# Kernel optimization log

Hardware: AMD Instinct MI355X
Metric: run time of the kernel (lower is better)

The kernel has to match this reference:

```python
import jax, jax.numpy as jnp
import numpy as np

NUM_HEADS = 8
IN_CH = 256  # C per branch; x has 2*C channels
DHW = (16, 16, 16)


def _proj(w, b, feat):
    # 1x1x1 Conv3d == per-voxel linear over channels. w: [Co, Ci], feat: [B, Ci, D, H, W]
    return jnp.einsum('oc,bcdhw->bodhw', w, feat) + b[None, :, None, None, None]


def _rope(n, dim):
    # matches rotary_embedding: returns [dim, n]
    inv_freq = 1.0 / (10000.0 ** (jnp.arange(0, dim, 2, dtype=jnp.float32) / dim))
    pos = jnp.linspace(-1.0, 1.0, n)
    sinusoid = pos[:, None] * inv_freq[None, :]          # [n, dim//2]
    emb = jnp.concatenate([jnp.sin(sinusoid), jnp.cos(sinusoid)], axis=-1)  # [n, dim]
    return emb.T                                          # [dim, n]


def setup_inputs() -> dict:
    key = jax.random.key(0)
    ks = jax.random.split(key, 5)
    D, H, W = DHW
    C = IN_CH
    s = 0.05
    return {
        'x': jax.random.normal(ks[0], (1, 2 * C, D, H, W), dtype=jnp.float32),
        'wq': jax.random.normal(ks[1], (C, C), dtype=jnp.float32) * s,
        'bq': jnp.zeros((C,), jnp.float32),
        'wk': jax.random.normal(ks[2], (C, C), dtype=jnp.float32) * s,
        'bk': jnp.zeros((C,), jnp.float32),
        'wv': jax.random.normal(ks[3], (C, C), dtype=jnp.float32) * s,
        'bv': jnp.zeros((C,), jnp.float32),
        'wo': jax.random.normal(ks[4], (2 * C, C), dtype=jnp.float32) * s,
        'bo': jnp.zeros((2 * C,), jnp.float32),
    }


def reference(x, wq, bq, wk, bk, wv, bv, wo, bo):
    qf, kvf = jnp.split(x, 2, axis=1)          # each [B, C, D, H, W]
    B, C, D, H, W = qf.shape
    hd = C // NUM_HEADS
    N = D * H * W
    q = _proj(wq, bq, qf).reshape(B, NUM_HEADS, hd, N)
    k = _proj(wk, bk, kvf).reshape(B, NUM_HEADS, hd, N)
    v = _proj(wv, bv, kvf).reshape(B, NUM_HEADS, hd, N)
    pe = _rope(N, hd)                           # [hd, N]
    q = q * pe[None, None]
    k = k * pe[None, None]
    attn = jnp.einsum('bhcn,bhcm->bhnm', q, k)  # note: no 1/sqrt(d) scaling, as in source
    attn = jax.nn.softmax(attn, axis=-1)
    out = jnp.einsum('bhnm,bhcm->bhcn', attn, v).reshape(B, C, D, H, W)
    return _proj(wo, bo, out + qf)              # [B, 2C, D, H, W]
```

## Files before the change

### kernel.cpp

```cpp
#include <hip/hip_runtime.h>
#include <hip/hip_bf16.h>

#define CIN 256
#define NV 4096
#define NHEAD 8
#define HD 32
#define NSPLIT 4
#define KSPAN (NV / NSPLIT)
#define KTILE 128
#define LOG2E 1.44269504088896340736f
#define LOG2_10K_16 0.8304820237218405f

typedef __attribute__((ext_vector_type(8))) short short8;
typedef __attribute__((ext_vector_type(4))) float f32x4;

static __device__ __forceinline__ unsigned short f2bf(float f) {
    union { float f; unsigned u; } v; v.f = f;
    unsigned r = v.u + 0x7fffu + ((v.u >> 16) & 1u);
    return (unsigned short)(r >> 16);
}
static __device__ __forceinline__ unsigned pk_bf2(float x0, float x1) {
    return __builtin_amdgcn_perm(__float_as_uint(x1), __float_as_uint(x0),
                                 0x07060302u);
}
static __device__ __forceinline__ float bflo(unsigned u) {
    return __uint_as_float(u << 16);
}
static __device__ __forceinline__ float bfhi(unsigned u) {
    return __uint_as_float(u & 0xffff0000u);
}

__global__ __launch_bounds__(256) void conv_w(
    const float* __restrict__ wq, const float* __restrict__ wk,
    const float* __restrict__ wv, const float* __restrict__ wo,
    unsigned short* __restrict__ Wb)
{
    int i = (blockIdx.x * 256 + threadIdx.x) * 4;
    if (i >= 327680) return;
    const float* src;
    int off = i;
    if (i < 65536) { src = wq; }
    else if (i < 131072) { src = wk; off = i - 65536; }
    else if (i < 196608) { src = wv; off = i - 131072; }
    else { src = wo; off = i - 196608; }
    float4 v = *(const float4*)&src[off];
    unsigned short pk[4] = {f2bf(v.x), f2bf(v.y), f2bf(v.z), f2bf(v.w)};
    *(uint2*)&Wb[i] = *(uint2*)pk;
}

__global__ __launch_bounds__(512) void qkv_fused(
    const float* __restrict__ x, const unsigned short* __restrict__ Wb,
    const float* __restrict__ bq, const float* __restrict__ bk,
    const float* __restrict__ bv,
    unsigned short* __restrict__ Qbf, unsigned short* __restrict__ Kbf,
    unsigned short* __restrict__ Vbf)
{
    const int which = blockIdx.z;
    const unsigned short* Wp = Wb + (size_t)which * 65536;
    const float* Bp = (which == 0) ? bq : (which == 1) ? bk : bv;
    const int cbase = (which == 0) ? 0 : CIN;

    const int n0 = blockIdx.x * 32;
    const int m0 = blockIdx.y * 128;
    const int t = threadIdx.x;

    __shared__ __align__(16) unsigned short Sbuf[32 * 264];

    {
        const int n = t & 31, cg = t >> 5;
#pragma unroll 4
        for (int cc = 0; cc < 16; cc += 2) {
            const int c = cg * 16 + cc;
            size_t off = (size_t)(cbase + c) * NV + n0 + n;
            *(unsigned*)&Sbuf[n * 264 + c] = pk_bf2(x[off], x[off + NV]);
        }
    }
    __syncthreads();

    const int w = t >> 6;
    const int lane = t & 63;
    const int ln = lane & 15;
    const int quad = lane >> 4;
    const int M = m0 + w * 16 + ln;

    f32x4 acc[2] = {};
    const unsigned short* Wrow = &Wp[(size_t)M * 256 + quad * 8];
    for (int k0 = 0; k0 < 256; k0 += 32) {
        short8 a = *(const short8*)&Wrow[k0];
        short8 b[2];
#pragma unroll
        for (int nt = 0; nt < 2; ++nt)
            b[nt] = *(const short8*)&Sbuf[(nt * 16 + ln) * 264 + k0 + quad * 8];
        if (which == 2) {
#pragma unroll
            for (int nt = 0; nt < 2; ++nt)
                acc[nt] = __builtin_amdgcn_mfma_f32_16x16x32_bf16(
                    b[nt], a, acc[nt], 0, 0, 0);
        } else {
#pragma unroll
            for (int nt = 0; nt < 2; ++nt)
                acc[nt] = __builtin_amdgcn_mfma_f32_16x16x32_bf16(
                    a, b[nt], acc[nt], 0, 0, 0);
        }
    }
    __syncthreads();

    if (which == 2) {
        const int cl = w * 16 + ln;
        const float bias = Bp[m0 + cl];
#pragma unroll
        for (int nt = 0; nt < 2; ++nt) {
            unsigned short pk4[4];
#pragma unroll
            for (int r = 0; r < 4; ++r) pk4[r] = f2bf(acc[nt][r] + bias);
            *(uint2*)&Sbuf[cl * 40 + nt * 16 + quad * 4] = *(uint2*)pk4;
        }
        __syncthreads();
        {
            const int cl2 = t >> 2, q = t & 3;
            uint2 lo = *(const uint2*)&Sbuf[cl2 * 40 + q * 4];
            uint2 hi = *(const uint2*)&Sbuf[cl2 * 40 + 16 + q * 4];
            uint4 v;
            v.x = lo.x; v.y = lo.y; v.z = hi.x; v.w = hi.y;
            *(uint4*)&Vbf[(size_t)(m0 + cl2) * NV + n0 + q * 8] = v;
        }
    } else {
        const int mb = m0 + w * 16 + quad * 4;
        const int cb = mb & 31;
        const float qscale = (which == 0) ? LOG2E : 1.0f;
        float bias[4], invf[4];
#pragma unroll
        for (int r = 0; r < 4; ++r) {
            bias[r] = Bp[mb + r];
            invf[r] = __builtin_amdgcn_exp2f(
                -(float)((cb + r) & 15) * LOG2_10K_16);
        }
        const bool use_sin = (cb < 16);
        const int ml = w * 16 + quad * 4;
#pragma unroll
        for (int nt = 0; nt < 2; ++nt) {
            const int n = n0 + nt * 16 + ln;
            const float pos = (float)n * (2.0f / 4095.0f) - 1.0f;
#pragma unroll
            for (int r = 0; r < 4; ++r) {
                float ang = pos * invf[r];
                float f = (use_sin ? __sinf(ang) : __cosf(ang)) * qscale;
                Sbuf[(nt * 16 + ln) * 264 + ml + r] =
                    f2bf((acc[nt][r] + bias[r]) * f);
            }
        }
        __syncthreads();
        unsigned short* dst = (which == 0) ? Qbf : Kbf;
        const int h0 = m0 >> 5;
        {
            const int hh = t >> 7;
            const int n = (t >> 2) & 31;
            const int cw = t & 3;
            uint4 v = *(const uint4*)&Sbuf[n * 264 + hh * 32 + cw * 8];
            *(uint4*)&dst[((size_t)(h0 + hh) * NV + n0 + n) * HD + cw * 8] = v;
        }
    }
}

__global__ __launch_bounds__(256, 4) void attn_mfma(
    const unsigned short* __restrict__ Qbf,
    const unsigned short* __restrict__ Kbf,
    const unsigned short* __restrict__ Vbf,
    unsigned short* __restrict__ Opartb, float* __restrict__ Lpart)
{
    const int h = blockIdx.y;
    const int q0 = blockIdx.x * 64;
    const int z = blockIdx.z;
    const int kbase = z * KSPAN;
    const int t = threadIdx.x;
    const int w = t >> 6;
    const int lane = t & 63;
    const int ln = lane & 15;
    const int quad = lane >> 4;

    __shared__ __align__(16) unsigned short Ks[2][2 * 2048];
    __shared__ __align__(16) unsigned short Vs[2][2 * 2048];

    const short8 qa = *(const short8*)
        &Qbf[((size_t)h * NV + q0 + w * 16 + ln) * HD + quad * 8];

    const unsigned short* Kh = Kbf + (size_t)h * NV * HD;
    const unsigned short* Vh = Vbf + (size_t)h * HD * NV;

    const int cv = t >> 3;
    const unsigned short* gsrcV = Vh + (size_t)cv * NV + ((t & 7) ^ (cv & 7)) * 8;
    const int kv = t >> 2;
    const unsigned short* gsrcK =
        Kh + (size_t)kv * HD + ((t & 3) ^ (kv & 3)) * 8;

    f32x4 oacc[2] = {};
    f32x4 lacc = {};
    const short vone = (short)0x3F80;
    const short8 vones = {vone, vone, vone, vone, vone, vone, vone, vone};

#pragma unroll
    for (int sblk = 0; sblk < 2; ++sblk) {
        __builtin_amdgcn_global_load_lds(
            (const __attribute__((address_space(1))) unsigned int*)(gsrcK +
                (size_t)(kbase + sblk * 64) * HD),
            (__attribute__((address_space(3))) unsigned int*)
                (&Ks[0][sblk * 2048] + t * 8), 16, 0, 0);
        __builtin_amdgcn_global_load_lds(
            (const __attribute__((address_space(1))) unsigned int*)(gsrcV +
                kbase + sblk * 64),
            (__attribute__((address_space(3))) unsigned int*)
                (&Vs[0][sblk * 2048] + t * 8), 16, 0, 0);
    }
    __syncthreads();

    const int sgk = (quad ^ (ln & 3)) * 8;
    for (int i = 0; i < KSPAN / KTILE; ++i) {
        const int kb = kbase + i * KTILE;
        const int buf = i & 1;

        if (i + 1 < KSPAN / KTILE) {
#pragma unroll
            for (int sblk = 0; sblk < 2; ++sblk) {
                __builtin_amdgcn_global_load_lds(
                    (const __attribute__((address_space(1))) unsigned int*)
                        (gsrcK + (size_t)(kb + KTILE + sblk * 64) * HD),
                    (__attribute__((address_space(3))) unsigned int*)
                        (&Ks[buf ^ 1][sblk * 2048] + t * 8), 16, 0, 0);
                __builtin_amdgcn_global_load_lds(
                    (const __attribute__((address_space(1))) unsigned int*)
                        (gsrcV + kb + KTILE + sblk * 64),
                    (__attribute__((address_space(3))) unsigned int*)
                        (&Vs[buf ^ 1][sblk * 2048] + t * 8), 16, 0, 0);
            }
        }

#pragma unroll
        for (int sblk = 0; sblk < 2; ++sblk) {
            f32x4 s[4];
#pragma unroll
            for (int ct = 0; ct < 4; ++ct) {
                const short8 kf = *(const short8*)
                    &Ks[buf][sblk * 2048 + (ct * 16 + ln) * 32 + sgk];
                f32x4 z4 = {0.f, 0.f, 0.f, 0.f};
                s[ct] = __builtin_amdgcn_mfma_f32_16x16x32_bf16(kf, qa, z4,
                                                                0, 0, 0);
            }

            float p[4][4];
#pragma unroll
            for (int ct = 0; ct < 4; ++ct)
#pragma unroll
                for (int r = 0; r < 4; ++r)
                    p[ct][r] = __builtin_amdgcn_exp2f(s[ct][r]);

#pragma unroll
            for (int h2 = 0; h2 < 2; ++h2) {
                short8 pa;
                unsigned* pau = (unsigned*)&pa;
                pau[0] = pk_bf2(p[2 * h2][0], p[2 * h2][1]);
                pau[1] = pk_bf2(p[2 * h2][2], p[2 * h2][3]);
                pau[2] = pk_bf2(p[2 * h2 + 1][0], p[2 * h2 + 1][1]);
                pau[3] = pk_bf2(p[2 * h2 + 1][2], p[2 * h2 + 1][3]);
                lacc = __builtin_amdgcn_mfma_f32_16x16x32_bf16(pa, vones, lacc,
                                                               0, 0, 0);
#pragma unroll
                for (int ctile = 0; ctile < 2; ++ctile) {
                    const int cA = ctile * 16 + ln;
                    const short8 vb = *(const short8*)
                        &Vs[buf][sblk * 2048 + cA * 64 +
                                 (((h2 * 4 + quad) ^ (cA & 7)) * 8)];
                    oacc[ctile] = __builtin_amdgcn_mfma_f32_16x16x32_bf16(
                        pa, vb, oacc[ctile], 0, 0, 0);
                }
            }
        }
        __syncthreads();
    }

    unsigned short* Oz = Opartb + (size_t)z * CIN * NV;
    float* Lz = Lpart + (size_t)z * NHEAD * NV;
    if (ln == 0) {
#pragma unroll
        for (int r = 0; r < 4; ++r)
            Lz[(size_t)h * NV + q0 + w * 16 + quad * 4 + r] = lacc[r];
    }
#pragma unroll
    for (int ctile = 0; ctile < 2; ++ctile) {
        uint2 st;
        st.x = pk_bf2(oacc[ctile][0], oacc[ctile][1]);
        st.y = pk_bf2(oacc[ctile][2], oacc[ctile][3]);
        *(uint2*)&Oz[(size_t)(h * HD + ctile * 16 + ln) * NV + q0 + w * 16 +
                     quad * 4] = st;
    }
}

__global__ __launch_bounds__(512) void out_fused(
    const float* __restrict__ x,
    const unsigned short* __restrict__ Opartb,
    const float* __restrict__ Lpart,
    const unsigned short* __restrict__ Wob, const float* __restrict__ bo,
    float* __restrict__ out)
{
    const int n0 = blockIdx.x * 32;
    const int m0 = blockIdx.y * 128;
    const int t = threadIdx.x;

    __shared__ __align__(16) unsigned short Ys[32 * 264];

    {
        const int n2 = (t & 15) * 2;
        const int grp = t >> 4;
        const int h = grp >> 2;
        const size_t lo = (size_t)h * NV + n0 + n2;
        float l0 = 0.f, l1 = 0.f;
#pragma unroll
        for (int zz = 0; zz < NSPLIT; ++zz) {
            l0 += Lpart[(size_t)zz * NHEAD * NV + lo];
            l1 += Lpart[(size_t)zz * NHEAD * NV + lo + 1];
        }
        const float rl0 = __builtin_amdgcn_rcpf(l0);
        const float rl1 = __builtin_amdgcn_rcpf(l1);
#pragma unroll
        for (int i = 0; i < 8; ++i) {
            const int c = grp * 8 + i;
            size_t off = (size_t)c * NV + n0 + n2;
            float s0 = 0.f, s1 = 0.f;
#pragma unroll
            for (int zz = 0; zz < NSPLIT; ++zz) {
                unsigned o = *(const unsigned*)&Opartb[(size_t)zz * CIN * NV + off];
                s0 += bflo(o);
                s1 += bfhi(o);
            }
            float2 x2 = *(const float2*)&x[off];
            Ys[n2 * 264 + c] = f2bf(s0 * rl0 + x2.x);
            Ys[(n2 + 1) * 264 + c] = f2bf(s1 * rl1 + x2.y);
        }
    }
    __syncthreads();

    const int w = t >> 6;
    const int lane = t & 63;
    const int ln = lane & 15;
    const int quad = lane >> 4;
    const int M = m0 + w * 16 + ln;

    const unsigned short* Wrow = &Wob[(size_t)M * 256 + quad * 8];
    f32x4 acc[2] = {};
    for (int k0 = 0; k0 < 256; k0 += 32) {
        short8 a = *(const short8*)&Wrow[k0];
        short8 b[2];
#pragma unroll
        for (int nt = 0; nt < 2; ++nt)
            b[nt] = *(const short8*)&Ys[(nt * 16 + ln) * 264 + k0 + quad * 8];
#pragma unroll
        for (int nt = 0; nt < 2; ++nt)
            acc[nt] = __builtin_amdgcn_mfma_f32_16x16x32_bf16(
                a, b[nt], acc[nt], 0, 0, 0);
    }

    const int mb = m0 + w * 16 + quad * 4;
    float bias[4];
#pragma unroll
    for (int r = 0; r < 4; ++r) bias[r] = bo[mb + r];
#pragma unroll
    for (int nt = 0; nt < 2; ++nt)
#pragma unroll
        for (int r = 0; r < 4; ++r)
            out[(size_t)(mb + r) * NV + n0 + nt * 16 + ln] =
                acc[nt][r] + bias[r];
}

extern "C" void kernel_launch(void* const* d_in, const int* in_sizes, int n_in,
                              void* d_out, int out_size, void* d_ws,
                              size_t ws_size, hipStream_t stream)
{
    const float* x  = (const float*)d_in[0];
    const float* wq = (const float*)d_in[1];
    const float* bq = (const float*)d_in[2];
    const float* wk = (const float*)d_in[3];
    const float* bk = (const float*)d_in[4];
    const float* wv = (const float*)d_in[5];
    const float* bv = (const float*)d_in[6];
    const float* wo = (const float*)d_in[7];
    const float* bo = (const float*)d_in[8];
    float* out = (float*)d_out;

    unsigned short* Wb  = (unsigned short*)d_ws;
    unsigned short* Qbf = Wb + 327680;
    unsigned short* Kbf = Qbf + (size_t)CIN * NV;
    unsigned short* Vbf = Kbf + (size_t)CIN * NV;
    float* Lpart = (float*)(Vbf + (size_t)CIN * NV);
    unsigned short* Opartb =
        (unsigned short*)(Lpart + NSPLIT * (size_t)NHEAD * NV);

    conv_w<<<dim3(320), 256, 0, stream>>>(wq, wk, wv, wo, Wb);
    qkv_fused<<<dim3(128, 2, 3), 512, 0, stream>>>(
        x, Wb, bq, bk, bv, Qbf, Kbf, Vbf);
    attn_mfma<<<dim3(NV / 64, NHEAD, NSPLIT), 256, 0, stream>>>(
        Qbf, Kbf, Vbf, Opartb, Lpart);
    out_fused<<<dim3(128, 4), 512, 0, stream>>>(
        x, Opartb, Lpart, Wb + 196608, bo, out);
}
```

Baseline: 120.9 us.

## Fuse weight bf16 conversion into GEMMs and double query tile per attention block

```diff
diff --git a/kernel.cpp b/kernel.cpp
--- a/kernel.cpp
+++ b/kernel.cpp
@@ -30,33 +30,16 @@
     return __uint_as_float(u & 0xffff0000u);
 }
 
-__global__ __launch_bounds__(256) void conv_w(
-    const float* __restrict__ wq, const float* __restrict__ wk,
-    const float* __restrict__ wv, const float* __restrict__ wo,
-    unsigned short* __restrict__ Wb)
-{
-    int i = (blockIdx.x * 256 + threadIdx.x) * 4;
-    if (i >= 327680) return;
-    const float* src;
-    int off = i;
-    if (i < 65536) { src = wq; }
-    else if (i < 131072) { src = wk; off = i - 65536; }
-    else if (i < 196608) { src = wv; off = i - 131072; }
-    else { src = wo; off = i - 196608; }
-    float4 v = *(const float4*)&src[off];
-    unsigned short pk[4] = {f2bf(v.x), f2bf(v.y), f2bf(v.z), f2bf(v.w)};
-    *(uint2*)&Wb[i] = *(uint2*)pk;
-}
-
 __global__ __launch_bounds__(512) void qkv_fused(
-    const float* __restrict__ x, const unsigned short* __restrict__ Wb,
-    const float* __restrict__ bq, const float* __restrict__ bk,
-    const float* __restrict__ bv,
+    const float* __restrict__ x,
+    const float* __restrict__ wq, const float* __restrict__ bq,
+    const float* __restrict__ wk, const float* __restrict__ bk,
+    const float* __restrict__ wv, const float* __restrict__ bv,
     unsigned short* __restrict__ Qbf, unsigned short* __restrict__ Kbf,
     unsigned short* __restrict__ Vbf)
 {
     const int which = blockIdx.z;
-    const unsigned short* Wp = Wb + (size_t)which * 65536;
+    const float* Wp = (which == 0) ? wq : (which == 1) ? wk : wv;
     const float* Bp = (which == 0) ? bq : (which == 1) ? bk : bv;
     const int cbase = (which == 0) ? 0 : CIN;
 
@@ -84,9 +67,16 @@
     const int M = m0 + w * 16 + ln;
 
     f32x4 acc[2] = {};
-    const unsigned short* Wrow = &Wp[(size_t)M * 256 + quad * 8];
+    const float* Wrow = &Wp[(size_t)M * 256 + quad * 8];
     for (int k0 = 0; k0 < 256; k0 += 32) {
-        short8 a = *(const short8*)&Wrow[k0];
+        float4 a0 = *(const float4*)&Wrow[k0];
+        float4 a1 = *(const float4*)&Wrow[k0 + 4];
+        short8 a;
+        unsigned* au = (unsigned*)&a;
+        au[0] = pk_bf2(a0.x, a0.y);
+        au[1] = pk_bf2(a0.z, a0.w);
+        au[2] = pk_bf2(a1.x, a1.y);
+        au[3] = pk_bf2(a1.z, a1.w);
         short8 b[2];
 #pragma unroll
         for (int nt = 0; nt < 2; ++nt)
@@ -169,7 +159,7 @@
     unsigned short* __restrict__ Opartb, float* __restrict__ Lpart)
 {
     const int h = blockIdx.y;
-    const int q0 = blockIdx.x * 64;
+    const int q0 = blockIdx.x * 128;
     const int z = blockIdx.z;
     const int kbase = z * KSPAN;
     const int t = threadIdx.x;
@@ -181,8 +171,11 @@
     __shared__ __align__(16) unsigned short Ks[2][2 * 2048];
     __shared__ __align__(16) unsigned short Vs[2][2 * 2048];
 
-    const short8 qa = *(const short8*)
-        &Qbf[((size_t)h * NV + q0 + w * 16 + ln) * HD + quad * 8];
+    short8 qa[2];
+#pragma unroll
+    for (int s = 0; s < 2; ++s)
+        qa[s] = *(const short8*)
+            &Qbf[((size_t)h * NV + q0 + s * 64 + w * 16 + ln) * HD + quad * 8];
 
     const unsigned short* Kh = Kbf + (size_t)h * NV * HD;
     const unsigned short* Vh = Vbf + (size_t)h * HD * NV;
@@ -191,10 +184,10 @@
     const unsigned short* gsrcV = Vh + (size_t)cv * NV + ((t & 7) ^ (cv & 7)) * 8;
     const int kv = t >> 2;
     const unsigned short* gsrcK =
-        Kh + (size_t)kv * HD + ((t & 3) ^ (kv & 3)) * 8;
-
-    f32x4 oacc[2] = {};
-    f32x4 lacc = {};
+        Kh + (size_t)kv * HD + ((t & 3) ^ ((kv >> 1) & 3)) * 8;
+
+    f32x4 oacc[2][2] = {};
+    f32x4 lacc[2] = {};
     const short vone = (short)0x3F80;
     const short8 vones = {vone, vone, vone, vone, vone, vone, vone, vone};
 
@@ -213,7 +206,7 @@
     }
     __syncthreads();
 
-    const int sgk = (quad ^ (ln & 3)) * 8;
+    const int sgk = (quad ^ ((ln >> 1) & 3)) * 8;
     for (int i = 0; i < KSPAN / KTILE; ++i) {
         const int kb = kbase + i * KTILE;
         const int buf = i & 1;
@@ -236,41 +229,62 @@
 
 #pragma unroll
         for (int sblk = 0; sblk < 2; ++sblk) {
-            f32x4 s[4];
-#pragma unroll
-            for (int ct = 0; ct < 4; ++ct) {
-                const short8 kf = *(const short8*)
+            short8 kfr[4];
+#pragma unroll
+            for (int ct = 0; ct < 4; ++ct)
+                kfr[ct] = *(const short8*)
                     &Ks[buf][sblk * 2048 + (ct * 16 + ln) * 32 + sgk];
-                f32x4 z4 = {0.f, 0.f, 0.f, 0.f};
-                s[ct] = __builtin_amdgcn_mfma_f32_16x16x32_bf16(kf, qa, z4,
-                                                                0, 0, 0);
+
+            unsigned paP[2][8];
+#pragma unroll
+            for (int s = 0; s < 2; ++s) {
+                f32x4 sv[4];
+#pragma unroll
+                for (int ct = 0; ct < 4; ++ct) {
+                    f32x4 z4 = {0.f, 0.f, 0.f, 0.f};
+                    sv[ct] = __builtin_amdgcn_mfma_f32_16x16x32_bf16(
+                        kfr[ct], qa[s], z4, 0, 0, 0);
+                }
+                float p[4][4];
+#pragma unroll
+                for (int ct = 0; ct < 4; ++ct)
+#pragma unroll
+                    for (int r = 0; r < 4; ++r)
+                        p[ct][r] = __builtin_amdgcn_exp2f(sv[ct][r]);
+#pragma unroll
+                for (int h2 = 0; h2 < 2; ++h2) {
+                    paP[s][h2 * 4 + 0] = pk_bf2(p[2 * h2][0], p[2 * h2][1]);
+                    paP[s][h2 * 4 + 1] = pk_bf2(p[2 * h2][2], p[2 * h2][3]);
+                    paP[s][h2 * 4 + 2] =
+                        pk_bf2(p[2 * h2 + 1][0], p[2 * h2 + 1][1]);
+                    paP[s][h2 * 4 + 3] =
+                        pk_bf2(p[2 * h2 + 1][2], p[2 * h2 + 1][3]);
+                }
             }
 
-            float p[4][4];
-#pragma unroll
-            for (int ct = 0; ct < 4; ++ct)
-#pragma unroll
-                for (int r = 0; r < 4; ++r)
-                    p[ct][r] = __builtin_amdgcn_exp2f(s[ct][r]);
-
 #pragma unroll
             for (int h2 = 0; h2 < 2; ++h2) {
-                short8 pa;
-                unsigned* pau = (unsigned*)&pa;
-                pau[0] = pk_bf2(p[2 * h2][0], p[2 * h2][1]);
-                pau[1] = pk_bf2(p[2 * h2][2], p[2 * h2][3]);
-                pau[2] = pk_bf2(p[2 * h2 + 1][0], p[2 * h2 + 1][1]);
-                pau[3] = pk_bf2(p[2 * h2 + 1][2], p[2 * h2 + 1][3]);
-                lacc = __builtin_amdgcn_mfma_f32_16x16x32_bf16(pa, vones, lacc,
-                                                               0, 0, 0);
+                short8 pa[2];
+#pragma unroll
+                for (int s = 0; s < 2; ++s) {
+                    unsigned* pau = (unsigned*)&pa[s];
+                    pau[0] = paP[s][h2 * 4 + 0];
+                    pau[1] = paP[s][h2 * 4 + 1];
+                    pau[2] = paP[s][h2 * 4 + 2];
+                    pau[3] = paP[s][h2 * 4 + 3];
+                    lacc[s] = __builtin_amdgcn_mfma_f32_16x16x32_bf16(
+                        pa[s], vones, lacc[s], 0, 0, 0);
+                }
 #pragma unroll
                 for (int ctile = 0; ctile < 2; ++ctile) {
                     const int cA = ctile * 16 + ln;
                     const short8 vb = *(const short8*)
                         &Vs[buf][sblk * 2048 + cA * 64 +
                                  (((h2 * 4 + quad) ^ (cA & 7)) * 8)];
-                    oacc[ctile] = __builtin_amdgcn_mfma_f32_16x16x32_bf16(
-                        pa, vb, oacc[ctile], 0, 0, 0);
+#pragma unroll
+                    for (int s = 0; s < 2; ++s)
+                        oacc[s][ctile] = __builtin_amdgcn_mfma_f32_16x16x32_bf16(
+                            pa[s], vb, oacc[s][ctile], 0, 0, 0);
                 }
             }
         }
@@ -279,18 +293,22 @@
 
     unsigned short* Oz = Opartb + (size_t)z * CIN * NV;
     float* Lz = Lpart + (size_t)z * NHEAD * NV;
-    if (ln == 0) {
-#pragma unroll
-        for (int r = 0; r < 4; ++r)
-            Lz[(size_t)h * NV + q0 + w * 16 + quad * 4 + r] = lacc[r];
-    }
-#pragma unroll
-    for (int ctile = 0; ctile < 2; ++ctile) {
-        uint2 st;
-        st.x = pk_bf2(oacc[ctile][0], oacc[ctile][1]);
-        st.y = pk_bf2(oacc[ctile][2], oacc[ctile][3]);
-        *(uint2*)&Oz[(size_t)(h * HD + ctile * 16 + ln) * NV + q0 + w * 16 +
-                     quad * 4] = st;
+#pragma unroll
+    for (int s = 0; s < 2; ++s) {
+        const int qs = q0 + s * 64 + w * 16;
+        if (ln == 0) {
+#pragma unroll
+            for (int r = 0; r < 4; ++r)
+                Lz[(size_t)h * NV + qs + quad * 4 + r] = lacc[s][r];
+        }
+#pragma unroll
+        for (int ctile = 0; ctile < 2; ++ctile) {
+            uint2 st;
+            st.x = pk_bf2(oacc[s][ctile][0], oacc[s][ctile][1]);
+            st.y = pk_bf2(oacc[s][ctile][2], oacc[s][ctile][3]);
+            *(uint2*)&Oz[(size_t)(h * HD + ctile * 16 + ln) * NV + qs +
+                         quad * 4] = st;
+        }
     }
 }
 
@@ -298,7 +316,7 @@
     const float* __restrict__ x,
     const unsigned short* __restrict__ Opartb,
     const float* __restrict__ Lpart,
-    const unsigned short* __restrict__ Wob, const float* __restrict__ bo,
+    const float* __restrict__ wo, const float* __restrict__ bo,
     float* __restrict__ out)
 {
     const int n0 = blockIdx.x * 32;
@@ -344,10 +362,17 @@
     const int quad = lane >> 4;
     const int M = m0 + w * 16 + ln;
 
-    const unsigned short* Wrow = &Wob[(size_t)M * 256 + quad * 8];
+    const float* Wrow = &wo[(size_t)M * 256 + quad * 8];
     f32x4 acc[2] = {};
     for (int k0 = 0; k0 < 256; k0 += 32) {
-        short8 a = *(const short8*)&Wrow[k0];
+        float4 a0 = *(const float4*)&Wrow[k0];
+        float4 a1 = *(const float4*)&Wrow[k0 + 4];
+        short8 a;
+        unsigned* au = (unsigned*)&a;
+        au[0] = pk_bf2(a0.x, a0.y);
+        au[1] = pk_bf2(a0.z, a0.w);
+        au[2] = pk_bf2(a1.x, a1.y);
+        au[3] = pk_bf2(a1.z, a1.w);
         short8 b[2];
 #pragma unroll
         for (int nt = 0; nt < 2; ++nt)
@@ -385,19 +410,17 @@
     const float* bo = (const float*)d_in[8];
     float* out = (float*)d_out;
 
-    unsigned short* Wb  = (unsigned short*)d_ws;
-    unsigned short* Qbf = Wb + 327680;
+    unsigned short* Qbf = (unsigned short*)d_ws;
     unsigned short* Kbf = Qbf + (size_t)CIN * NV;
     unsigned short* Vbf = Kbf + (size_t)CIN * NV;
     float* Lpart = (float*)(Vbf + (size_t)CIN * NV);
     unsigned short* Opartb =
         (unsigned short*)(Lpart + NSPLIT * (size_t)NHEAD * NV);
 
-    conv_w<<<dim3(320), 256, 0, stream>>>(wq, wk, wv, wo, Wb);
     qkv_fused<<<dim3(128, 2, 3), 512, 0, stream>>>(
-        x, Wb, bq, bk, bv, Qbf, Kbf, Vbf);
-    attn_mfma<<<dim3(NV / 64, NHEAD, NSPLIT), 256, 0, stream>>>(
+        x, wq, bq, wk, bk, wv, bv, Qbf, Kbf, Vbf);
+    attn_mfma<<<dim3(NV / 128, NHEAD, NSPLIT), 256, 0, stream>>>(
         Qbf, Kbf, Vbf, Opartb, Lpart);
     out_fused<<<dim3(128, 4), 512, 0, stream>>>(
-        x, Opartb, Lpart, Wb + 196608, bo, out);
-}
+        x, Opartb, Lpart, wo, bo, out);
+}
```

Result: slower. 123.6 us (+2.2%).
